# Optimization experiments

Hardware: AMD Instinct MI355X
Metric: run time of the kernel (lower is better)

The kernel has to match this reference:

```python
import jax, jax.numpy as jnp
import numpy as np
from jax import lax

B, CIN, H, W = 32, 128, 64, 64
COUT, K, NK, HID = 128, 3, 4, 32
TEMP = 34.0
PAD = 1


def setup_inputs() -> dict:
    key = jax.random.key(0)
    k1, k2, k3, k4 = jax.random.split(key, 4)
    x = jax.random.normal(k1, (B, CIN, H, W), dtype=jnp.float32)
    fc1_w = jax.random.normal(k2, (HID, CIN), dtype=jnp.float32) * (2.0 / CIN) ** 0.5
    fc2_w = jax.random.normal(k3, (NK, HID), dtype=jnp.float32) * (2.0 / HID) ** 0.5
    fc2_b = jnp.zeros((NK,), dtype=jnp.float32)
    weight = jax.random.normal(k4, (NK, COUT, CIN, K, K), dtype=jnp.float32) * 0.05
    bias = jnp.zeros((NK, COUT), dtype=jnp.float32)
    return {"x": x, "fc1_w": fc1_w, "fc2_w": fc2_w, "fc2_b": fc2_b,
            "weight": weight, "bias": bias}


def _per_sample_conv(xi, wi):
    # xi: [CIN, H, W], wi: [COUT, CIN, K, K]
    out = lax.conv_general_dilated(
        xi[None], wi,
        window_strides=(1, 1),
        padding=[(PAD, PAD), (PAD, PAD)],
        dimension_numbers=("NCHW", "OIHW", "NCHW"))
    return out[0]  # [COUT, H', W']


def reference(x, fc1_w, fc2_w, fc2_b, weight, bias):
    # attention: global avg pool -> 1x1 conv (matmul) -> relu -> 1x1 conv -> softmax
    context = jnp.mean(x, axis=(2, 3))                      # [B, CIN]
    hid = jax.nn.relu(context @ fc1_w.T)                    # [B, HID]
    logits = hid @ fc2_w.T + fc2_b                          # [B, NK]
    att = jax.nn.softmax(logits / TEMP, axis=1)             # [B, NK]
    # aggregate per-sample kernels and biases
    agg_w = jnp.einsum("bk,koihw->boihw", att, weight)      # [B, COUT, CIN, K, K]
    agg_b = att @ bias                                      # [B, COUT]
    # per-sample convolution (equivalent to the groups=B trick in torch)
    out = jax.vmap(_per_sample_conv)(x, agg_w)              # [B, COUT, H, W]
    return out + agg_b[:, :, None, None]
```

## Files before the change

kernel.cpp:

```cpp
#include <hip/hip_runtime.h>

#define B_    32
#define CIN_  128
#define H_    64
#define W_    64
#define COUT_ 128
#define NK_   4
#define HID_  32
#define TEMP_ 34.0f

typedef short bf16x8 __attribute__((ext_vector_type(8)));
typedef float f32x16 __attribute__((ext_vector_type(16)));

__device__ __forceinline__ short f2bf(float f) {
    union { float f; unsigned u; } c; c.f = f;
    unsigned r = (c.u + 0x7FFFu + ((c.u >> 16) & 1u)) >> 16;
    return (short)r;
}

__global__ __launch_bounds__(64) void k_context(const float* __restrict__ x,
                                                float* __restrict__ ctx) {
    const int bc = blockIdx.x;
    const float* p = x + (size_t)bc * (H_ * W_);
    const int lane = threadIdx.x;
    float s = 0.f;
    for (int i = lane * 4; i < H_ * W_; i += 64 * 4) {
        float4 v = *(const float4*)(p + i);
        s += v.x + v.y + v.z + v.w;
    }
    for (int off = 32; off > 0; off >>= 1) s += __shfl_down(s, off, 64);
    if (lane == 0) ctx[bc] = s * (1.0f / (H_ * W_));
}

__global__ __launch_bounds__(256) void k_aggw(const float* __restrict__ ctx,
        const float* __restrict__ fc1w, const float* __restrict__ fc2w,
        const float* __restrict__ fc2b, const float* __restrict__ bias,
        const float* __restrict__ weight, short* __restrict__ aggwt,
        float* __restrict__ aggb) {
    __shared__ float hidp[8][32];
    __shared__ float shid[32];
    __shared__ float satt[NK_];
    __shared__ float sbuf[2304];
    const int t = threadIdx.x;
    const int blk = blockIdx.x;
    const int b = blk >> 6;
    const int co0 = (blk & 63) * 2;
    {
        const int hh = t & 31, part = t >> 5;
        const float* c  = ctx + b * CIN_ + part * 16;
        const float* f1 = fc1w + hh * CIN_ + part * 16;
        float s = 0.f;
#pragma unroll
        for (int j = 0; j < 16; ++j) s += c[j] * f1[j];
        hidp[part][hh] = s;
    }
    __syncthreads();
    if (t < 32) {
        float s = 0.f;
#pragma unroll
        for (int p = 0; p < 8; ++p) s += hidp[p][t];
        shid[t] = fmaxf(s, 0.f);
    }
    __syncthreads();
    if (t == 0) {
        float lg[NK_]; float mx = -1e30f;
#pragma unroll
        for (int k = 0; k < NK_; ++k) {
            float s = fc2b[k];
            for (int hh = 0; hh < HID_; ++hh) s += shid[hh] * fc2w[k * HID_ + hh];
            lg[k] = s / TEMP_; mx = fmaxf(mx, lg[k]);
        }
        float den = 0.f;
#pragma unroll
        for (int k = 0; k < NK_; ++k) { lg[k] = expf(lg[k] - mx); den += lg[k]; }
        const float rd = 1.0f / den;
#pragma unroll
        for (int k = 0; k < NK_; ++k) satt[k] = lg[k] * rd;
    }
    __syncthreads();
    const float a0 = satt[0], a1 = satt[1], a2 = satt[2], a3 = satt[3];

    if ((t & 127) == 0) {
        const int co = co0 + (t >> 7);
        aggb[b * COUT_ + co] = a0 * bias[co] + a1 * bias[COUT_ + co]
                             + a2 * bias[2 * COUT_ + co] + a3 * bias[3 * COUT_ + co];
    }

    const size_t kstride = (size_t)COUT_ * CIN_ * 9;
    const float* W0 = weight + (size_t)co0 * (CIN_ * 9);
#pragma unroll
    for (int jj = 0; jj < 3; ++jj) {
        const int i4 = jj * 256 + t;
        if (i4 < 576) {
            const float4 w0 = *(const float4*)(W0 + i4 * 4);
            const float4 w1 = *(const float4*)(W0 + kstride + i4 * 4);
            const float4 w2 = *(const float4*)(W0 + 2 * kstride + i4 * 4);
            const float4 w3 = *(const float4*)(W0 + 3 * kstride + i4 * 4);
            float4 r;
            r.x = a0 * w0.x + a1 * w1.x + a2 * w2.x + a3 * w3.x;
            r.y = a0 * w0.y + a1 * w1.y + a2 * w2.y + a3 * w3.y;
            r.z = a0 * w0.z + a1 * w1.z + a2 * w2.z + a3 * w3.z;
            r.w = a0 * w0.w + a1 * w1.w + a2 * w2.w + a3 * w3.w;
            *(float4*)(&sbuf[i4 * 4]) = r;
        }
    }
    __syncthreads();
#pragma unroll
    for (int jj = 0; jj < 2; ++jj) {
        const int g = jj * 256 + t;
        if (g < 288) {
            const int coL = (g >= 144) ? 1 : 0;
            const int gg = g - coL * 144;
            const int r  = gg >> 4;
            const int oc = gg & 15;
            const int co = co0 + coL;
            bf16x8 v;
#pragma unroll
            for (int e = 0; e < 8; ++e)
                v[e] = f2bf(sbuf[(coL * 128 + oc * 8 + e) * 9 + r]);
            short* dst = aggwt
                + ((size_t)(((b * 4 + (co >> 5)) * 9 + r) * 8 + (oc >> 1)) * 512)
                + ((co & 31) * 2 + (oc & 1)) * 8;
            *(bf16x8*)dst = v;
        }
    }
}

#define RBY 8448
#define RSH 4224
__global__ __launch_bounds__(256, 2) void k_conv(const float* __restrict__ x,
        const short* __restrict__ aggwt, const float* __restrict__ aggb,
        float* __restrict__ out) {
    __shared__ short xt[6 * RSH];
    const int tid = threadIdx.x;
    const int blk = blockIdx.x;
    const int b = blk & 31;
    const int h0 = (blk >> 5) * 4;
    const int lane = tid & 63;
    const int wv = tid >> 6;
    const int l31 = lane & 31;
    const int lane5 = lane >> 5;

    if (tid < 96) {
        const int row = tid >> 4;
        const int q = tid & 15;
        const int cl = (q < 8) ? q : (512 + q);
        *(int4*)(&xt[row * RSH + cl * 8]) = make_int4(0, 0, 0, 0);
    }

    f32x16 acc[8];
#pragma unroll
    for (int t = 0; t < 8; ++t)
#pragma unroll
        for (int k = 0; k < 16; ++k) acc[t][k] = 0.f;

    const short* Ap = aggwt + (size_t)(b * 4 + wv) * (9 * 8 * 512)
                            + (size_t)(l31 * 2 + lane5) * 8;

    for (int half = 0; half < 2; ++half) {
        const int cib = half * 64;
#pragma unroll
        for (int k = 0; k < 12; ++k) {
            const int task = k * 4 + wv;
            const int row = task >> 3;
            const int g = task & 7;
            const int in_h = h0 - 1 + row;
            bf16x8 v = (bf16x8){0, 0, 0, 0, 0, 0, 0, 0};
            if (in_h >= 0 && in_h < H_) {
                const float* gp = x + (((size_t)b * CIN_ + cib + g * 8) * H_ + in_h) * W_ + lane;
                float f[8];
#pragma unroll
                for (int j = 0; j < 8; ++j) f[j] = gp[j * (H_ * W_)];
#pragma unroll
                for (int j = 0; j < 8; ++j) v[j] = f2bf(f[j]);
            }
            *(bf16x8*)(&xt[row * RSH + ((lane + 1) * 8 + ((g + lane) & 7)) * 8]) = v;
        }
        __syncthreads();

#pragma unroll
        for (int kcl = 0; kcl < 4; ++kcl) {
            const int kc = half * 4 + kcl;
            bf16x8 av[9];
#pragma unroll
            for (int r = 0; r < 9; ++r)
                av[r] = *(const bf16x8*)(Ap + ((size_t)(r * 8 + kc)) * 512);
#pragma unroll
            for (int ir = 0; ir < 6; ++ir) {
                bf16x8 bv[2][3];
#pragma unroll
                for (int i = 0; i < 2; ++i)
#pragma unroll
                    for (int kw = 0; kw < 3; ++kw) {
                        const int s = i * 32 + l31 + kw;
                        const int off = 16 * ((2 * kcl + lane5 + s - 1) & 7);
                        bv[i][kw] = *(const bf16x8*)((const char*)xt + ir * RBY + s * 128 + off);
                    }
#pragma unroll
                for (int orr = 0; orr < 4; ++orr) {
                    if (orr <= ir && ir <= orr + 2) {
                        const int kh = ir - orr;
#pragma unroll
                        for (int i = 0; i < 2; ++i)
#pragma unroll
                            for (int kw = 0; kw < 3; ++kw)
                                acc[orr * 2 + i] = __builtin_amdgcn_mfma_f32_32x32x16_bf16(
                                    av[kh * 3 + kw], bv[i][kw], acc[orr * 2 + i], 0, 0, 0);
                    }
                }
            }
        }
        if (half == 0) __syncthreads();
    }

    const float* ab = aggb + b * COUT_;
#pragma unroll
    for (int orr = 0; orr < 4; ++orr) {
#pragma unroll
        for (int i = 0; i < 2; ++i) {
            const int hh = h0 + orr;
            const int w = i * 32 + l31;
            float* op = out + ((size_t)b * COUT_ * H_ + hh) * W_ + w;
            const f32x16 a = acc[orr * 2 + i];
#pragma unroll
            for (int reg = 0; reg < 16; ++reg) {
                const int co = wv * 32 + (reg & 3) + 8 * (reg >> 2) + 4 * lane5;
                op[(size_t)co * (H_ * W_)] = a[reg] + ab[co];
            }
        }
    }
}

extern "C" void kernel_launch(void* const* d_in, const int* in_sizes, int n_in,
                              void* d_out, int out_size, void* d_ws, size_t ws_size,
                              hipStream_t stream) {
    const float* x    = (const float*)d_in[0];
    const float* fc1w = (const float*)d_in[1];
    const float* fc2w = (const float*)d_in[2];
    const float* fc2b = (const float*)d_in[3];
    const float* wgt  = (const float*)d_in[4];
    const float* bias = (const float*)d_in[5];
    float* out = (float*)d_out;

    char* ws = (char*)d_ws;
    float* ctx   = (float*)(ws + 0);
    float* aggb  = (float*)(ws + 16384);
    short* aggwt = (short*)(ws + 65536);

    k_context<<<dim3(B_ * CIN_), dim3(64), 0, stream>>>(x, ctx);
    k_aggw<<<dim3(B_ * (COUT_ / 2)), dim3(256), 0, stream>>>(
        ctx, fc1w, fc2w, fc2b, bias, wgt, aggwt, aggb);
    k_conv<<<dim3(B_ * (H_ / 4)), dim3(256), 0, stream>>>(x, aggwt, aggb, out);
}
```

Before: 169.3 us.

## Pipeline second-half input staging across MFMA channel chunks

Instead of loading both 64-channel halves of the input tile in separate phases, the kernel loads the first half up front. It then streams the second half in slices: global loads for each slice are issued before that chunk's MFMA work, and the slice is written into shared memory after a barrier. The goal is to hide global-load latency behind tensor-core compute and remove the bulk reload stall. MFMA sections are also wrapped in s_setprio to raise wave priority. In exchange there are more barriers and extra registers held across the compute loop, which could hurt occupancy.

```diff
diff --git a/kernel.cpp b/kernel.cpp
--- a/kernel.cpp
+++ b/kernel.cpp
@@ -157,60 +157,91 @@
     const short* Ap = aggwt + (size_t)(b * 4 + wv) * (9 * 8 * 512)
                             + (size_t)(l31 * 2 + lane5) * 8;
 
-    for (int half = 0; half < 2; ++half) {
-        const int cib = half * 64;
-#pragma unroll
-        for (int k = 0; k < 12; ++k) {
-            const int task = k * 4 + wv;
-            const int row = task >> 3;
-            const int g = task & 7;
-            const int in_h = h0 - 1 + row;
-            bf16x8 v = (bf16x8){0, 0, 0, 0, 0, 0, 0, 0};
-            if (in_h >= 0 && in_h < H_) {
-                const float* gp = x + (((size_t)b * CIN_ + cib + g * 8) * H_ + in_h) * W_ + lane;
-                float f[8];
-#pragma unroll
-                for (int j = 0; j < 8; ++j) f[j] = gp[j * (H_ * W_)];
-#pragma unroll
-                for (int j = 0; j < 8; ++j) v[j] = f2bf(f[j]);
-            }
-            *(bf16x8*)(&xt[row * RSH + ((lane + 1) * 8 + ((g + lane) & 7)) * 8]) = v;
-        }
-        __syncthreads();
-
-#pragma unroll
-        for (int kcl = 0; kcl < 4; ++kcl) {
-            const int kc = half * 4 + kcl;
-            bf16x8 av[9];
-#pragma unroll
-            for (int r = 0; r < 9; ++r)
-                av[r] = *(const bf16x8*)(Ap + ((size_t)(r * 8 + kc)) * 512);
-#pragma unroll
-            for (int ir = 0; ir < 6; ++ir) {
-                bf16x8 bv[2][3];
-#pragma unroll
-                for (int i = 0; i < 2; ++i)
-#pragma unroll
-                    for (int kw = 0; kw < 3; ++kw) {
-                        const int s = i * 32 + l31 + kw;
-                        const int off = 16 * ((2 * kcl + lane5 + s - 1) & 7);
-                        bv[i][kw] = *(const bf16x8*)((const char*)xt + ir * RBY + s * 128 + off);
-                    }
-#pragma unroll
-                for (int orr = 0; orr < 4; ++orr) {
-                    if (orr <= ir && ir <= orr + 2) {
-                        const int kh = ir - orr;
-#pragma unroll
-                        for (int i = 0; i < 2; ++i)
-#pragma unroll
-                            for (int kw = 0; kw < 3; ++kw)
-                                acc[orr * 2 + i] = __builtin_amdgcn_mfma_f32_32x32x16_bf16(
-                                    av[kh * 3 + kw], bv[i][kw], acc[orr * 2 + i], 0, 0, 0);
-                    }
-                }
-            }
-        }
-        if (half == 0) __syncthreads();
+#pragma unroll
+    for (int k = 0; k < 12; ++k) {
+        const int task = k * 4 + wv;
+        const int row = task >> 3;
+        const int g = task & 7;
+        const int in_h = h0 - 1 + row;
+        bf16x8 v = (bf16x8){0, 0, 0, 0, 0, 0, 0, 0};
+        if (in_h >= 0 && in_h < H_) {
+            const float* gp = x + (((size_t)b * CIN_ + g * 8) * H_ + in_h) * W_ + lane;
+            float f[8];
+#pragma unroll
+            for (int j = 0; j < 8; ++j) f[j] = gp[j * (H_ * W_)];
+#pragma unroll
+            for (int j = 0; j < 8; ++j) v[j] = f2bf(f[j]);
+        }
+        *(bf16x8*)(&xt[row * RSH + ((lane + 1) * 8 + ((g + lane) & 7)) * 8]) = v;
+    }
+    __syncthreads();
+
+#pragma unroll
+    for (int kc = 0; kc < 8; ++kc) {
+        float sf[3][8];
+        if (kc < 4) {
+#pragma unroll
+            for (int k = 0; k < 3; ++k) {
+                const int task = k * 4 + wv;
+                const int row = task >> 1;
+                const int j = task & 1;
+                const int in_h = h0 - 1 + row;
+                if (in_h >= 0 && in_h < H_) {
+                    const float* gp = x + (((size_t)b * CIN_ + 64 + (2 * kc + j) * 8) * H_
+                                           + in_h) * W_ + lane;
+#pragma unroll
+                    for (int jj = 0; jj < 8; ++jj) sf[k][jj] = gp[jj * (H_ * W_)];
+                }
+            }
+        }
+        bf16x8 av[9];
+#pragma unroll
+        for (int r = 0; r < 9; ++r)
+            av[r] = *(const bf16x8*)(Ap + ((size_t)(r * 8 + kc)) * 512);
+        const int kcl = kc & 3;
+        __builtin_amdgcn_s_setprio(1);
+#pragma unroll
+        for (int ir = 0; ir < 6; ++ir) {
+            bf16x8 bv[2][3];
+#pragma unroll
+            for (int i = 0; i < 2; ++i)
+#pragma unroll
+                for (int kw = 0; kw < 3; ++kw) {
+                    const int s = i * 32 + l31 + kw;
+                    const int off = 16 * ((2 * kcl + lane5 + s - 1) & 7);
+                    bv[i][kw] = *(const bf16x8*)((const char*)xt + ir * RBY + s * 128 + off);
+                }
+#pragma unroll
+            for (int orr = 0; orr < 4; ++orr) {
+                if (orr <= ir && ir <= orr + 2) {
+                    const int kh = ir - orr;
+#pragma unroll
+                    for (int i = 0; i < 2; ++i)
+#pragma unroll
+                        for (int kw = 0; kw < 3; ++kw)
+                            acc[orr * 2 + i] = __builtin_amdgcn_mfma_f32_32x32x16_bf16(
+                                av[kh * 3 + kw], bv[i][kw], acc[orr * 2 + i], 0, 0, 0);
+                }
+            }
+        }
+        __builtin_amdgcn_s_setprio(0);
+        if (kc <= 4) __syncthreads();
+        if (kc < 4) {
+#pragma unroll
+            for (int k = 0; k < 3; ++k) {
+                const int task = k * 4 + wv;
+                const int row = task >> 1;
+                const int j = task & 1;
+                const int in_h = h0 - 1 + row;
+                const int g = 2 * kc + j;
+                bf16x8 v = (bf16x8){0, 0, 0, 0, 0, 0, 0, 0};
+                if (in_h >= 0 && in_h < H_) {
+#pragma unroll
+                    for (int jj = 0; jj < 8; ++jj) v[jj] = f2bf(sf[k][jj]);
+                }
+                *(bf16x8*)(&xt[row * RSH + ((lane + 1) * 8 + ((g + lane) & 7)) * 8]) = v;
+            }
+        }
     }
 
     const float* ab = aggb + b * COUT_;
```

New measurement: 165.4 us. 2.3% less time.
